# Kernel tuning notes

Hardware: AMD Instinct MI355X
Metric: run time of the kernel (lower is better)

## Reference

```python
import jax, jax.numpy as jnp
import numpy as np

HEADS = 8
BN_EPS = 1e-5


def setup_inputs() -> dict:
    B, S, D = 8, 1024, 512
    key = jax.random.key(0)
    ks = jax.random.split(key, 4)
    x = jax.random.normal(ks[0], (B, S, D), dtype=jnp.float32)
    scale = 0.02
    Wq = jax.random.normal(ks[1], (D, D), dtype=jnp.float32) * scale
    Wk = jax.random.normal(ks[2], (D, D), dtype=jnp.float32) * scale
    Wv = jax.random.normal(ks[3], (D, D), dtype=jnp.float32) * scale
    zeros = jnp.zeros((D,), dtype=jnp.float32)
    return {
        "x": x,
        "Wq": Wq, "bq": zeros,
        "Wk": Wk, "bk": zeros,
        "Wv": Wv, "bv": zeros,
        "gamma": jnp.ones((D,), dtype=jnp.float32),
        "beta": zeros,
    }


def reference(x, Wq, bq, Wk, bk, Wv, bv, gamma, beta):
    # x: [B, S, D]
    B, S, D = x.shape
    H = HEADS
    dh = D // H

    Q = jax.nn.relu(jnp.einsum('bsd,de->bse', x, Wq) + bq).reshape(B, S, H, dh)
    K = jax.nn.relu(jnp.einsum('bsd,de->bse', x, Wk) + bk).reshape(B, S, H, dh)
    V = jax.nn.relu(jnp.einsum('bsd,de->bse', x, Wv) + bv).reshape(B, S, H, dh)

    # torch split(dim=2)+cat(dim=0) == per-head batched attention; scores [B,H,q,k]
    scores = jnp.einsum('bqhd,bkhd->bhqk', Q, K) / jnp.sqrt(jnp.float32(dh))
    # NOTE: original uses F.softmax(output, dim=1) on [H*B, S, S]; dim=1 is the
    # QUERY axis (non-standard), i.e. axis 2 of [b,h,q,k].
    attn = jax.nn.softmax(scores, axis=2)
    # dropout omitted (deterministic / eval mode)
    out = jnp.einsum('bhqk,bkhd->bqhd', attn, V).reshape(B, S, D)

    y = out + x  # residual

    # BatchNorm1d (training mode): per-channel stats over (B, S), biased var
    mean = jnp.mean(y, axis=(0, 1))
    var = jnp.mean(jnp.square(y - mean), axis=(0, 1))
    y = (y - mean) * jax.lax.rsqrt(var + BN_EPS) * gamma + beta
    return y
```

## Files before the change

kernel.cpp:

```cpp
#include <hip/hip_runtime.h>
#include <hip/hip_bf16.h>
#include <math.h>

typedef __bf16 bf16;
typedef __bf16 bf16x8 __attribute__((ext_vector_type(8)));
typedef float floatx4 __attribute__((ext_vector_type(4)));

#define NB 8
#define NS 1024
#define ND 512
#define NH 8
#define NDH 64
#define NBH 64
#define MROWS 8192
#define N3 1536

#define GLD16(src, dst)                                                            \
    __builtin_amdgcn_global_load_lds(                                              \
        (const __attribute__((address_space(1))) void*)(src),                      \
        (__attribute__((address_space(3))) void*)(dst), 16, 0, 0)

static __device__ __forceinline__ floatx4 mfma16(bf16x8 a, bf16x8 b, floatx4 c) {
    return __builtin_amdgcn_mfma_f32_16x16x32_bf16(a, b, c, 0, 0, 0);
}

static __device__ __forceinline__ unsigned pack2(float lo, float hi) {
    union { bf16 h[2]; unsigned u; } u;
    u.h[0] = (bf16)lo; u.h[1] = (bf16)hi;
    return u.u;
}

static __device__ __forceinline__ void plane32(unsigned &a, unsigned &b) {
    asm volatile("v_permlane32_swap_b32 %0, %1" : "+v"(a), "+v"(b));
}
static __device__ __forceinline__ void plane16(unsigned &a, unsigned &b) {
    asm volatile("v_permlane16_swap_b32 %0, %1" : "+v"(a), "+v"(b));
}

__global__ void zero_f32(float* p, int n) {
    int i = blockIdx.x * 256 + threadIdx.x;
    if (i < n) p[i] = 0.f;
}

__global__ void convert_x(const float* __restrict__ x, bf16* __restrict__ xb) {
    int i = (blockIdx.x * 256 + threadIdx.x) * 8;
    float4 a = *(const float4*)&x[i];
    float4 b = *(const float4*)&x[i + 4];
    bf16 o[8] = {(bf16)a.x, (bf16)a.y, (bf16)a.z, (bf16)a.w,
                 (bf16)b.x, (bf16)b.y, (bf16)b.z, (bf16)b.w};
    *(bf16x8*)&xb[i] = *(bf16x8*)o;
}

__global__ void convert_w(const float* __restrict__ Wq, const float* __restrict__ Wk,
                          const float* __restrict__ Wv, bf16* __restrict__ Wb) {
    __shared__ float t[32][33];
    int mat = blockIdx.z;
    const float* W = mat == 0 ? Wq : (mat == 1 ? Wk : Wv);
    int d0 = blockIdx.x * 32, e0 = blockIdx.y * 32;
    int tx = threadIdx.x, ty = threadIdx.y;
#pragma unroll
    for (int i = 0; i < 4; i++) t[ty * 4 + i][tx] = W[(d0 + ty * 4 + i) * ND + e0 + tx];
    __syncthreads();
#pragma unroll
    for (int i = 0; i < 4; i++)
        Wb[(mat * ND + e0 + ty * 4 + i) * ND + d0 + tx] = (bf16)t[tx][ty * 4 + i];
}

__launch_bounds__(256)
__global__ void gemm1(const bf16* __restrict__ xb, const bf16* __restrict__ Wb,
                      const float* __restrict__ bq, const float* __restrict__ bk,
                      const float* __restrict__ bv, bf16* __restrict__ QKV) {
    __shared__ __align__(16) bf16 As[128 * 64];
    __shared__ __align__(16) bf16 Bs[128 * 64];
    int t = threadIdx.x, lane = t & 63, w = t >> 6;
    int wr = w >> 1, wc = w & 1;
    int lr = lane & 15, lg = lane >> 4;
    int row0 = blockIdx.x * 128, col0 = blockIdx.y * 128;
    int srow = t >> 3, sj = t & 7;
    floatx4 acc[4][4] = {};
    for (int k0 = 0; k0 < ND; k0 += 64) {
        __syncthreads();
#pragma unroll
        for (int it = 0; it < 4; it++) {
            int row = it * 32 + srow;
            int j = sj ^ (row & 7);
            GLD16(&xb[(size_t)(row0 + row) * ND + k0 + j * 8], &As[(it * 256 + w * 64) * 8]);
            GLD16(&Wb[(size_t)(col0 + row) * ND + k0 + j * 8], &Bs[(it * 256 + w * 64) * 8]);
        }
        __syncthreads();
        bf16x8 af[2][4], bfr[2][4];
#pragma unroll
        for (int ks = 0; ks < 2; ks++) {
#pragma unroll
            for (int mt = 0; mt < 4; mt++)
                af[ks][mt] = *(const bf16x8*)&As[(wr * 64 + mt * 16 + lr) * 64 +
                                                 ((ks * 4 + lg) ^ (lr & 7)) * 8];
#pragma unroll
            for (int nt = 0; nt < 4; nt++)
                bfr[ks][nt] = *(const bf16x8*)&Bs[(wc * 64 + nt * 16 + lr) * 64 +
                                                  ((ks * 4 + lg) ^ (lr & 7)) * 8];
        }
#pragma unroll
        for (int ks = 0; ks < 2; ks++)
#pragma unroll
            for (int mt = 0; mt < 4; mt++)
#pragma unroll
                for (int nt = 0; nt < 4; nt++)
                    acc[mt][nt] = mfma16(af[ks][mt], bfr[ks][nt], acc[mt][nt]);
    }
#pragma unroll
    for (int mt = 0; mt < 4; mt++)
#pragma unroll
        for (int nt = 0; nt < 4; nt++) {
            int col = col0 + wc * 64 + nt * 16 + lr;
            float bias = col < 512 ? bq[col] : (col < 1024 ? bk[col - 512] : bv[col - 1024]);
#pragma unroll
            for (int r = 0; r < 4; r++) {
                int row = row0 + wr * 64 + mt * 16 + lg * 4 + r;
                float v = acc[mt][nt][r] + bias;
                v = v > 0.f ? v : 0.f;
                QKV[(size_t)row * N3 + col] = (bf16)v;
            }
        }
}

__launch_bounds__(256)
__global__ void attn_colsum(const bf16* __restrict__ QKV, float* __restrict__ rc_arr) {
    __shared__ __align__(16) bf16 Qs[128 * 64];
    int bh = blockIdx.x, b = bh >> 3, h = bh & 7;
    int k0 = blockIdx.y * 128;
    int t = threadIdx.x, lane = t & 63, w = t >> 6;
    int lr = lane & 15, lg = lane >> 4;
    int srow = t >> 3, sj = t & 7;
    bf16x8 kf[2][2];
#pragma unroll
    for (int tt = 0; tt < 2; tt++)
#pragma unroll
        for (int s = 0; s < 2; s++)
            kf[tt][s] = *(const bf16x8*)&QKV[(size_t)(b * NS + k0 + w * 32 + tt * 16 + lr) * N3 +
                                             512 + h * NDH + s * 32 + lg * 8];
    floatx4 csum[2] = {};
    const floatx4 zf = {};
    for (int qc = 0; qc < 8; qc++) {
        __syncthreads();
#pragma unroll
        for (int it = 0; it < 4; it++) {
            int row = it * 32 + srow;
            int j = sj ^ (row & 7);
            GLD16(&QKV[(size_t)(b * NS + qc * 128 + row) * N3 + h * NDH + j * 8],
                  &Qs[(it * 256 + w * 64) * 8]);
        }
        __syncthreads();
#pragma unroll
        for (int qt = 0; qt < 8; qt++) {
            bf16x8 qb0 = *(const bf16x8*)&Qs[(qt * 16 + lr) * 64 + (lg ^ (lr & 7)) * 8];
            bf16x8 qb1 = *(const bf16x8*)&Qs[(qt * 16 + lr) * 64 + ((4 + lg) ^ (lr & 7)) * 8];
#pragma unroll
            for (int tt = 0; tt < 2; tt++) {
                floatx4 a = mfma16(kf[tt][0], qb0, zf);
                a = mfma16(kf[tt][1], qb1, a);
#pragma unroll
                for (int r = 0; r < 4; r++) csum[tt][r] += __expf(a[r] * 0.125f);
            }
        }
    }
#pragma unroll
    for (int tt = 0; tt < 2; tt++)
#pragma unroll
        for (int r = 0; r < 4; r++) {
            float v = csum[tt][r];
            v += __shfl_xor(v, 1);
            v += __shfl_xor(v, 2);
            v += __shfl_xor(v, 4);
            v += __shfl_xor(v, 8);
            csum[tt][r] = v;
        }
    if (lr == 0) {
#pragma unroll
        for (int tt = 0; tt < 2; tt++)
#pragma unroll
            for (int r = 0; r < 4; r++)
                rc_arr[bh * NS + k0 + w * 32 + tt * 16 + lg * 4 + r] = 1.f / csum[tt][r];
    }
}

__global__ void transpose_v(const bf16* __restrict__ QKV, const float* __restrict__ rc_arr,
                            bf16* __restrict__ Vt) {
    __shared__ __align__(16) bf16 tile[64][72];
    int bh = blockIdx.x, b = bh >> 3, h = bh & 7;
    int s0 = blockIdx.y * 64;
    int t = threadIdx.x;
    int sl = t >> 3, cg = t & 7;
#pragma unroll
    for (int rr = 0; rr < 64; rr += 32)
        *(bf16x8*)&tile[rr + sl][cg * 8] =
            *(const bf16x8*)&QKV[(size_t)(b * NS + s0 + rr + sl) * N3 + 1024 + h * NDH + cg * 8];
    __syncthreads();
    int dl = t >> 3, sg = t & 7;
    float4 rc0 = *(const float4*)&rc_arr[bh * NS + s0 + sg * 8];
    float4 rc1 = *(const float4*)&rc_arr[bh * NS + s0 + sg * 8 + 4];
    float rcv[8] = {rc0.x, rc0.y, rc0.z, rc0.w, rc1.x, rc1.y, rc1.z, rc1.w};
#pragma unroll
    for (int rr = 0; rr < 64; rr += 32) {
        bf16 tmp[8];
#pragma unroll
        for (int j = 0; j < 8; j++)
            tmp[j] = (bf16)((float)tile[sg * 8 + j][rr + dl] * rcv[j]);
        *(bf16x8*)&Vt[(size_t)(bh * NDH + rr + dl) * NS + s0 + sg * 8] = *(bf16x8*)tmp;
    }
}

__launch_bounds__(256)
__global__ void attn_fused(const bf16* __restrict__ QKV, const bf16* __restrict__ Vt,
                           const float* __restrict__ x, float* __restrict__ y,
                           float* __restrict__ bnSum, float* __restrict__ bnSumSq) {
    __shared__ __align__(16) bf16 Ks[128 * 64];
    __shared__ __align__(16) bf16 Vs[64 * 128];
    int bh = blockIdx.x, b = bh >> 3, h = bh & 7;
    int q0 = blockIdx.y * 128;
    int t = threadIdx.x, lane = t & 63, w = t >> 6;
    int lr = lane & 15, lg = lane >> 4;
    bf16x8 qf[2][2];
#pragma unroll
    for (int n = 0; n < 2; n++)
#pragma unroll
        for (int s = 0; s < 2; s++)
            qf[n][s] = *(const bf16x8*)&QKV[(size_t)(b * NS + q0 + w * 32 + n * 16 + lr) * N3 +
                                            h * NDH + s * 32 + lg * 8];
    floatx4 oacc[2][4] = {};
    const floatx4 zf = {};
    int sKrow = t >> 3, sKj = t & 7;
    int sVrow = t >> 4, sVj = t & 15;
    for (int k0 = 0; k0 < NS; k0 += 128) {
        __syncthreads();
#pragma unroll
        for (int it = 0; it < 4; it++) {
            int rowK = it * 32 + sKrow;
            int jK = sKj ^ (rowK & 7);
            GLD16(&QKV[(size_t)(b * NS + k0 + rowK) * N3 + 512 + h * NDH + jK * 8],
                  &Ks[(it * 256 + w * 64) * 8]);
            int rowV = it * 16 + sVrow;
            int jV = sVj ^ (rowV & 7);
            GLD16(&Vt[(size_t)(bh * NDH + rowV) * NS + k0 + jV * 8],
                  &Vs[(it * 256 + w * 64) * 8]);
        }
        __syncthreads();
#pragma unroll
        for (int kt = 0; kt < 4; kt++) {
            bf16x8 kfr[2][2];
#pragma unroll
            for (int tt = 0; tt < 2; tt++)
#pragma unroll
                for (int s = 0; s < 2; s++)
                    kfr[tt][s] = *(const bf16x8*)&Ks[(kt * 32 + tt * 16 + lr) * 64 +
                                                     ((s * 4 + lg) ^ (lr & 7)) * 8];
            bf16x8 vf[4];
#pragma unroll
            for (int nt = 0; nt < 4; nt++)
                vf[nt] = *(const bf16x8*)&Vs[(nt * 16 + lr) * 128 +
                                             ((kt * 4 + lg) ^ (lr & 7)) * 8];
#pragma unroll
            for (int n = 0; n < 2; n++) {
                floatx4 s0 = mfma16(kfr[0][0], qf[n][0], zf);
                s0 = mfma16(kfr[0][1], qf[n][1], s0);
                floatx4 s1 = mfma16(kfr[1][0], qf[n][0], zf);
                s1 = mfma16(kfr[1][1], qf[n][1], s1);
                float e0[4], e1[4];
#pragma unroll
                for (int r = 0; r < 4; r++) {
                    e0[r] = __expf(s0[r] * 0.125f);
                    e1[r] = __expf(s1[r] * 0.125f);
                }
                unsigned A0 = pack2(e0[0], e0[1]);
                unsigned A1 = pack2(e0[2], e0[3]);
                unsigned B0 = pack2(e1[0], e1[1]);
                unsigned B1 = pack2(e1[2], e1[3]);
                plane32(A0, B0); plane16(A0, B0);
                plane32(A1, B1); plane16(A1, B1);
                union { unsigned u[4]; bf16x8 v; } af;
                af.u[0] = A0; af.u[1] = A1; af.u[2] = B0; af.u[3] = B1;
#pragma unroll
                for (int nt = 0; nt < 4; nt++)
                    oacc[n][nt] = mfma16(af.v, vf[nt], oacc[n][nt]);
            }
        }
    }
    float bs[4] = {}, bq2[4] = {};
#pragma unroll
    for (int n = 0; n < 2; n++)
#pragma unroll
        for (int nt = 0; nt < 4; nt++) {
            int d = nt * 16 + lr;
#pragma unroll
            for (int r = 0; r < 4; r++) {
                int q = q0 + w * 32 + n * 16 + lg * 4 + r;
                size_t idx = (size_t)(b * NS + q) * ND + h * NDH + d;
                float yv = oacc[n][nt][r] + x[idx];
                y[idx] = yv;
                bs[nt] += yv;
                bq2[nt] += yv * yv;
            }
        }
#pragma unroll
    for (int nt = 0; nt < 4; nt++) {
        float v = bs[nt], q2 = bq2[nt];
        v += __shfl_xor(v, 16); v += __shfl_xor(v, 32);
        q2 += __shfl_xor(q2, 16); q2 += __shfl_xor(q2, 32);
        if (lg == 0) {
            atomicAdd(&bnSum[h * NDH + nt * 16 + lr], v);
            atomicAdd(&bnSumSq[h * NDH + nt * 16 + lr], q2);
        }
    }
}

__global__ void bn_apply(float* __restrict__ y, const float* __restrict__ bnSum,
                         const float* __restrict__ bnSumSq, const float* __restrict__ gamma,
                         const float* __restrict__ beta) {
    int i = (blockIdx.x * 256 + threadIdx.x) * 4;
    int c = i & 511;
    float4 v = *(float4*)&y[i];
    float vv[4] = {v.x, v.y, v.z, v.w};
    float out[4];
#pragma unroll
    for (int j = 0; j < 4; j++) {
        float mean = bnSum[c + j] * (1.f / 8192.f);
        float var = bnSumSq[c + j] * (1.f / 8192.f) - mean * mean;
        float rstd = rsqrtf(var + 1e-5f);
        out[j] = (vv[j] - mean) * rstd * gamma[c + j] + beta[c + j];
    }
    *(float4*)&y[i] = make_float4(out[0], out[1], out[2], out[3]);
}

extern "C" void kernel_launch(void* const* d_in, const int* in_sizes, int n_in,
                              void* d_out, int out_size, void* d_ws, size_t ws_size,
                              hipStream_t stream) {
    const float* x  = (const float*)d_in[0];
    const float* Wq = (const float*)d_in[1];
    const float* bq = (const float*)d_in[2];
    const float* Wk = (const float*)d_in[3];
    const float* bk = (const float*)d_in[4];
    const float* Wv = (const float*)d_in[5];
    const float* bv = (const float*)d_in[6];
    const float* gamma = (const float*)d_in[7];
    const float* beta  = (const float*)d_in[8];
    float* y = (float*)d_out;

    char* ws = (char*)d_ws;
    const size_t WB_OFF  = 0;
    const size_t QKV_OFF = 2u << 20;
    const size_t VT_OFF  = QKV_OFF + (size_t)MROWS * N3 * 2;
    const size_t RC_OFF  = VT_OFF + (size_t)NBH * NDH * NS * 2;
    const size_t BN_OFF  = RC_OFF + (size_t)NBH * NS * 4;
    const size_t XB_OFF  = BN_OFF + (4u << 12);
    bf16*  Wb     = (bf16*)(ws + WB_OFF);
    bf16*  QKV    = (bf16*)(ws + QKV_OFF);
    bf16*  Vt     = (bf16*)(ws + VT_OFF);
    float* rc_arr = (float*)(ws + RC_OFF);
    float* bnSum  = (float*)(ws + BN_OFF);
    float* bnSumSq = bnSum + 512;
    bf16*  xb     = (bf16*)(ws + XB_OFF);

    zero_f32<<<4, 256, 0, stream>>>(bnSum, 1024);
    convert_x<<<2048, 256, 0, stream>>>(x, xb);
    convert_w<<<dim3(16, 16, 3), dim3(32, 8), 0, stream>>>(Wq, Wk, Wv, Wb);
    gemm1<<<dim3(64, 12), 256, 0, stream>>>(xb, Wb, bq, bk, bv, QKV);
    attn_colsum<<<dim3(64, 8), 256, 0, stream>>>(QKV, rc_arr);
    transpose_v<<<dim3(64, 16), 256, 0, stream>>>(QKV, rc_arr, Vt);
    attn_fused<<<dim3(64, 8), 256, 0, stream>>>(QKV, Vt, x, y, bnSum, bnSumSq);
    bn_apply<<<4096, 256, 0, stream>>>(y, bnSum, bnSumSq, gamma, beta);
}
```

Measured before the change: 98.44 us.

## Double-buffer attention LDS loads, fold softmax scale into K, swizzle blocks

Double-buffers the Q and K/V tiles in both attention kernels, issuing global-to-LDS loads for the next tile ahead of compute with explicit vmcnt waits and raw barriers. Folds the 1/sqrt(dh)·log2(e) scale into K in the GEMM epilogue so the inner loops use exp2f directly. Remaps block indices so the eight blocks of one batch-head are spread apart, and merges the BN-accumulator zeroing into convert_x to drop one launch. The doubled LDS use may lower occupancy, and rounding the pre-scaled K to bf16 slightly changes numerics.

```diff
diff --git a/kernel.cpp b/kernel.cpp
--- a/kernel.cpp
+++ b/kernel.cpp
@@ -14,6 +14,7 @@
 #define NBH 64
 #define MROWS 8192
 #define N3 1536
+#define KSCL 0.18033688f
 
 #define GLD16(src, dst)                                                            \
     __builtin_amdgcn_global_load_lds(                                              \
@@ -37,12 +38,17 @@
     asm volatile("v_permlane16_swap_b32 %0, %1" : "+v"(a), "+v"(b));
 }
 
-__global__ void zero_f32(float* p, int n) {
-    int i = blockIdx.x * 256 + threadIdx.x;
-    if (i < n) p[i] = 0.f;
-}
-
-__global__ void convert_x(const float* __restrict__ x, bf16* __restrict__ xb) {
+static __device__ __forceinline__ void barrier_np() {
+    __builtin_amdgcn_sched_barrier(0);
+    __builtin_amdgcn_s_barrier();
+    __builtin_amdgcn_sched_barrier(0);
+}
+
+__global__ void convert_x(const float* __restrict__ x, bf16* __restrict__ xb,
+                          float* __restrict__ bnSum) {
+    if (blockIdx.x == 0) {
+        ((float4*)bnSum)[threadIdx.x] = make_float4(0.f, 0.f, 0.f, 0.f);
+    }
     int i = (blockIdx.x * 256 + threadIdx.x) * 8;
     float4 a = *(const float4*)&x[i];
     float4 b = *(const float4*)&x[i + 4];
@@ -114,11 +120,13 @@
         for (int nt = 0; nt < 4; nt++) {
             int col = col0 + wc * 64 + nt * 16 + lr;
             float bias = col < 512 ? bq[col] : (col < 1024 ? bk[col - 512] : bv[col - 1024]);
+            float scl = (col >= 512 && col < 1024) ? KSCL : 1.0f;
 #pragma unroll
             for (int r = 0; r < 4; r++) {
                 int row = row0 + wr * 64 + mt * 16 + lg * 4 + r;
                 float v = acc[mt][nt][r] + bias;
                 v = v > 0.f ? v : 0.f;
+                v *= scl;
                 QKV[(size_t)row * N3 + col] = (bf16)v;
             }
         }
@@ -126,9 +134,12 @@
 
 __launch_bounds__(256)
 __global__ void attn_colsum(const bf16* __restrict__ QKV, float* __restrict__ rc_arr) {
-    __shared__ __align__(16) bf16 Qs[128 * 64];
-    int bh = blockIdx.x, b = bh >> 3, h = bh & 7;
-    int k0 = blockIdx.y * 128;
+    __shared__ __align__(16) bf16 Qs[2][128 * 64];
+    int id = blockIdx.x;
+    int swz = (id & 7) * 64 + (id >> 3);
+    int bh = swz >> 3, kb = swz & 7;
+    int b = bh >> 3, h = bh & 7;
+    int k0 = kb * 128;
     int t = threadIdx.x, lane = t & 63, w = t >> 6;
     int lr = lane & 15, lg = lane >> 4;
     int srow = t >> 3, sj = t & 7;
@@ -139,30 +150,41 @@
         for (int s = 0; s < 2; s++)
             kf[tt][s] = *(const bf16x8*)&QKV[(size_t)(b * NS + k0 + w * 32 + tt * 16 + lr) * N3 +
                                              512 + h * NDH + s * 32 + lg * 8];
-    floatx4 csum[2] = {};
-    const floatx4 zf = {};
-    for (int qc = 0; qc < 8; qc++) {
-        __syncthreads();
+    auto stageQ = [&](int buf, int qc) {
 #pragma unroll
         for (int it = 0; it < 4; it++) {
             int row = it * 32 + srow;
             int j = sj ^ (row & 7);
             GLD16(&QKV[(size_t)(b * NS + qc * 128 + row) * N3 + h * NDH + j * 8],
-                  &Qs[(it * 256 + w * 64) * 8]);
-        }
-        __syncthreads();
+                  &Qs[buf][(it * 256 + w * 64) * 8]);
+        }
+    };
+    floatx4 csum[2] = {};
+    const floatx4 zf = {};
+    stageQ(0, 0);
+#pragma unroll 2
+    for (int qc = 0; qc < 8; qc++) {
+        int cur = qc & 1;
+        if (qc < 7) {
+            stageQ(cur ^ 1, qc + 1);
+            asm volatile("s_waitcnt vmcnt(4)" ::: "memory");
+        } else {
+            asm volatile("s_waitcnt vmcnt(0)" ::: "memory");
+        }
+        barrier_np();
 #pragma unroll
         for (int qt = 0; qt < 8; qt++) {
-            bf16x8 qb0 = *(const bf16x8*)&Qs[(qt * 16 + lr) * 64 + (lg ^ (lr & 7)) * 8];
-            bf16x8 qb1 = *(const bf16x8*)&Qs[(qt * 16 + lr) * 64 + ((4 + lg) ^ (lr & 7)) * 8];
+            bf16x8 qb0 = *(const bf16x8*)&Qs[cur][(qt * 16 + lr) * 64 + (lg ^ (lr & 7)) * 8];
+            bf16x8 qb1 = *(const bf16x8*)&Qs[cur][(qt * 16 + lr) * 64 + ((4 + lg) ^ (lr & 7)) * 8];
 #pragma unroll
             for (int tt = 0; tt < 2; tt++) {
                 floatx4 a = mfma16(kf[tt][0], qb0, zf);
                 a = mfma16(kf[tt][1], qb1, a);
 #pragma unroll
-                for (int r = 0; r < 4; r++) csum[tt][r] += __expf(a[r] * 0.125f);
+                for (int r = 0; r < 4; r++) csum[tt][r] += exp2f(a[r]);
             }
         }
+        barrier_np();
     }
 #pragma unroll
     for (int tt = 0; tt < 2; tt++)
@@ -214,10 +236,13 @@
 __global__ void attn_fused(const bf16* __restrict__ QKV, const bf16* __restrict__ Vt,
                            const float* __restrict__ x, float* __restrict__ y,
                            float* __restrict__ bnSum, float* __restrict__ bnSumSq) {
-    __shared__ __align__(16) bf16 Ks[128 * 64];
-    __shared__ __align__(16) bf16 Vs[64 * 128];
-    int bh = blockIdx.x, b = bh >> 3, h = bh & 7;
-    int q0 = blockIdx.y * 128;
+    __shared__ __align__(16) bf16 Ks[2][128 * 64];
+    __shared__ __align__(16) bf16 Vs[2][64 * 128];
+    int id = blockIdx.x;
+    int swz = (id & 7) * 64 + (id >> 3);
+    int bh = swz >> 3, qb = swz & 7;
+    int b = bh >> 3, h = bh & 7;
+    int q0 = qb * 128;
     int t = threadIdx.x, lane = t & 63, w = t >> 6;
     int lr = lane & 15, lg = lane >> 4;
     bf16x8 qf[2][2];
@@ -227,24 +252,34 @@
         for (int s = 0; s < 2; s++)
             qf[n][s] = *(const bf16x8*)&QKV[(size_t)(b * NS + q0 + w * 32 + n * 16 + lr) * N3 +
                                             h * NDH + s * 32 + lg * 8];
-    floatx4 oacc[2][4] = {};
-    const floatx4 zf = {};
     int sKrow = t >> 3, sKj = t & 7;
     int sVrow = t >> 4, sVj = t & 15;
-    for (int k0 = 0; k0 < NS; k0 += 128) {
-        __syncthreads();
+    auto stageKV = [&](int buf, int k0) {
 #pragma unroll
         for (int it = 0; it < 4; it++) {
             int rowK = it * 32 + sKrow;
             int jK = sKj ^ (rowK & 7);
             GLD16(&QKV[(size_t)(b * NS + k0 + rowK) * N3 + 512 + h * NDH + jK * 8],
-                  &Ks[(it * 256 + w * 64) * 8]);
+                  &Ks[buf][(it * 256 + w * 64) * 8]);
             int rowV = it * 16 + sVrow;
             int jV = sVj ^ (rowV & 7);
             GLD16(&Vt[(size_t)(bh * NDH + rowV) * NS + k0 + jV * 8],
-                  &Vs[(it * 256 + w * 64) * 8]);
-        }
-        __syncthreads();
+                  &Vs[buf][(it * 256 + w * 64) * 8]);
+        }
+    };
+    floatx4 oacc[2][4] = {};
+    const floatx4 zf = {};
+    stageKV(0, 0);
+#pragma unroll 2
+    for (int kb = 0; kb < 8; kb++) {
+        int cur = kb & 1;
+        if (kb < 7) {
+            stageKV(cur ^ 1, (kb + 1) * 128);
+            asm volatile("s_waitcnt vmcnt(8)" ::: "memory");
+        } else {
+            asm volatile("s_waitcnt vmcnt(0)" ::: "memory");
+        }
+        barrier_np();
 #pragma unroll
         for (int kt = 0; kt < 4; kt++) {
             bf16x8 kfr[2][2];
@@ -252,13 +287,13 @@
             for (int tt = 0; tt < 2; tt++)
 #pragma unroll
                 for (int s = 0; s < 2; s++)
-                    kfr[tt][s] = *(const bf16x8*)&Ks[(kt * 32 + tt * 16 + lr) * 64 +
-                                                     ((s * 4 + lg) ^ (lr & 7)) * 8];
+                    kfr[tt][s] = *(const bf16x8*)&Ks[cur][(kt * 32 + tt * 16 + lr) * 64 +
+                                                          ((s * 4 + lg) ^ (lr & 7)) * 8];
             bf16x8 vf[4];
 #pragma unroll
             for (int nt = 0; nt < 4; nt++)
-                vf[nt] = *(const bf16x8*)&Vs[(nt * 16 + lr) * 128 +
-                                             ((kt * 4 + lg) ^ (lr & 7)) * 8];
+                vf[nt] = *(const bf16x8*)&Vs[cur][(nt * 16 + lr) * 128 +
+                                                  ((kt * 4 + lg) ^ (lr & 7)) * 8];
 #pragma unroll
             for (int n = 0; n < 2; n++) {
                 floatx4 s0 = mfma16(kfr[0][0], qf[n][0], zf);
@@ -268,8 +303,8 @@
                 float e0[4], e1[4];
 #pragma unroll
                 for (int r = 0; r < 4; r++) {
-                    e0[r] = __expf(s0[r] * 0.125f);
-                    e1[r] = __expf(s1[r] * 0.125f);
+                    e0[r] = exp2f(s0[r]);
+                    e1[r] = exp2f(s1[r]);
                 }
                 unsigned A0 = pack2(e0[0], e0[1]);
                 unsigned A1 = pack2(e0[2], e0[3]);
@@ -284,6 +319,7 @@
                     oacc[n][nt] = mfma16(af.v, vf[nt], oacc[n][nt]);
             }
         }
+        barrier_np();
     }
     float bs[4] = {}, bq2[4] = {};
 #pragma unroll
@@ -360,12 +396,11 @@
     float* bnSumSq = bnSum + 512;
     bf16*  xb     = (bf16*)(ws + XB_OFF);
 
-    zero_f32<<<4, 256, 0, stream>>>(bnSum, 1024);
-    convert_x<<<2048, 256, 0, stream>>>(x, xb);
+    convert_x<<<2048, 256, 0, stream>>>(x, xb, bnSum);
     convert_w<<<dim3(16, 16, 3), dim3(32, 8), 0, stream>>>(Wq, Wk, Wv, Wb);
     gemm1<<<dim3(64, 12), 256, 0, stream>>>(xb, Wb, bq, bk, bv, QKV);
-    attn_colsum<<<dim3(64, 8), 256, 0, stream>>>(QKV, rc_arr);
+    attn_colsum<<<512, 256, 0, stream>>>(QKV, rc_arr);
     transpose_v<<<dim3(64, 16), 256, 0, stream>>>(QKV, rc_arr, Vt);
-    attn_fused<<<dim3(64, 8), 256, 0, stream>>>(QKV, Vt, x, y, bnSum, bnSumSq);
+    attn_fused<<<512, 256, 0, stream>>>(QKV, Vt, x, y, bnSum, bnSumSq);
     bn_apply<<<4096, 256, 0, stream>>>(y, bnSum, bnSumSq, gamma, beta);
 }
```

Result: slower. 107.4 us (+9.1%).
